# Kernel tuning notes

Hardware: AMD Instinct MI355X
Metric: run time of the kernel (lower is better)

Reference implementation:

```python
import jax, jax.numpy as jnp
import numpy as np

B, N_LAT, N_PAT = 32, 64, 4096
DIM_LAT = DIM_PAT = DIM_ATTN = 192
H = 6
HD = DIM_ATTN // H  # 32
SCALE = HD ** -0.5


def setup_inputs() -> dict:
    key = jax.random.key(0)
    ks = jax.random.split(key, 8)
    s = lambda fan_in: 1.0 / np.sqrt(fan_in)
    return {
        "x_latents": jax.random.normal(ks[0], (B, N_LAT, DIM_LAT), jnp.float32),
        "x_patches": jax.random.normal(ks[1], (B, N_PAT, DIM_PAT), jnp.float32),
        # weights stored [in, out] (torch Linear applies x @ W.T; math identical)
        "W_rv_lat": jax.random.uniform(ks[2], (DIM_LAT, 2 * DIM_ATTN), jnp.float32, -s(DIM_LAT), s(DIM_LAT)),
        "W_rv_pat": jax.random.uniform(ks[3], (DIM_PAT, 2 * DIM_ATTN), jnp.float32, -s(DIM_PAT), s(DIM_PAT)),
        "W_proj_lat": jax.random.uniform(ks[4], (DIM_ATTN, DIM_LAT), jnp.float32, -s(DIM_ATTN), s(DIM_ATTN)),
        "b_proj_lat": jax.random.uniform(ks[5], (DIM_LAT,), jnp.float32, -s(DIM_ATTN), s(DIM_ATTN)),
        "W_proj_pat": jax.random.uniform(ks[6], (DIM_ATTN, DIM_PAT), jnp.float32, -s(DIM_ATTN), s(DIM_ATTN)),
        "b_proj_pat": jax.random.uniform(ks[7], (DIM_PAT,), jnp.float32, -s(DIM_ATTN), s(DIM_ATTN)),
    }


def _split_rv(x, W, n):
    # x: [B, n, d_in] -> r, v each [B, H, n, HD]
    rv = (x @ W).reshape(x.shape[0], n, 2, H, HD)
    rv = jnp.transpose(rv, (2, 0, 3, 1, 4))  # [2, B, H, n, HD]
    return rv[0], rv[1]


def reference(x_latents, x_patches, W_rv_lat, W_rv_pat,
              W_proj_lat, b_proj_lat, W_proj_pat, b_proj_pat):
    r_lat, v_lat = _split_rv(x_latents, W_rv_lat, N_LAT)   # [B,H,N_lat,HD]
    r_pat, v_pat = _split_rv(x_patches, W_rv_pat, N_PAT)   # [B,H,N_pat,HD]

    # single score matrix, softmaxed along both axes (dropout = 0, eval mode)
    scores = jnp.einsum('bhld,bhpd->bhlp', r_lat, r_pat) * SCALE  # [B,H,N_lat,N_pat]
    attn = jax.nn.softmax(scores, axis=-1)    # row-wise (over patches)
    attn_T = jax.nn.softmax(scores, axis=-2)  # col-wise (over latents)

    out_lat = jnp.einsum('bhlp,bhpd->blhd', attn, v_pat).reshape(B, N_LAT, DIM_ATTN)
    out_pat = jnp.einsum('bhlp,bhld->bphd', attn_T, v_lat).reshape(B, N_PAT, DIM_ATTN)

    out_lat = out_lat @ W_proj_lat + b_proj_lat
    out_pat = out_pat @ W_proj_pat + b_proj_pat
    return out_lat, out_pat
```

## Files before the change

kernel.cpp:

```cpp
#include <hip/hip_runtime.h>

#define B_   32
#define NL_  64
#define NP_  4096
#define DIM_ 192
#define H_   6
#define HD_  32
#define PC_  128
#define NCH_ (NP_/PC_)
#define CPB_ 4
#define NSC_ (NCH_/CPB_)

typedef unsigned short u16;
typedef __attribute__((ext_vector_type(8))) short bf16x8;
typedef __attribute__((ext_vector_type(4))) short bf16x4;
typedef __attribute__((ext_vector_type(4))) float f32x4;

#define MFMA16(a,b,c) __builtin_amdgcn_mfma_f32_16x16x32_bf16(a,b,c,0,0,0)

__device__ __forceinline__ float bf2f(u16 s){ return __builtin_bit_cast(float,(unsigned)s<<16); }
__device__ __forceinline__ u16 f2bf(float f){
  unsigned u = __builtin_bit_cast(unsigned,f);
  return (u16)((u + 0x7FFFu + ((u>>16)&1u))>>16);
}

__global__ void k0_transpose(const float* __restrict__ W0, const float* __restrict__ W1,
                             const float* __restrict__ W2, const float* __restrict__ W3,
                             u16* __restrict__ T0, u16* __restrict__ T1,
                             u16* __restrict__ T2, u16* __restrict__ T3){
  int m = blockIdx.x >> 4, sub = blockIdx.x & 15;
  const float* src; u16* dst; int R, C;
  if      (m==0){src=W0;dst=T0;R=192;C=384;}
  else if (m==1){src=W1;dst=T1;R=192;C=384;}
  else if (m==2){src=W2;dst=T2;R=192;C=192;}
  else          {src=W3;dst=T3;R=192;C=192;}
  int total = R*C;
  for (int o = sub*256 + threadIdx.x; o < total; o += 16*256){
    int c = o / R, r = o - c*R;
    dst[o] = f2bf(src[r*C + c]);
  }
}

__global__ __launch_bounds__(256) void k_rv(const float* __restrict__ X,
    const u16* __restrict__ Wt, u16* __restrict__ R, u16* __restrict__ V,
    int Nseq, int nshift){
  __shared__ u16 As[128*200];
  __shared__ u16 Bs[64*200];
  const int t = threadIdx.x;
  const int m0 = blockIdx.x*128;
  const int lane = t & 63, w = t >> 6, g = lane >> 4, ln = lane & 15;
  const int srow = t >> 2, sc = (t & 3) * 8;
  const int bq = t & 3;
  const f32x4 ZF = {0.f,0.f,0.f,0.f};

  #pragma unroll
  for (int rr = 0; rr < 128; rr += 64){
    #pragma unroll
    for (int k0 = 0; k0 < 192; k0 += 32){
      float4 x0 = *(const float4*)&X[(size_t)(m0 + rr + srow)*192 + k0 + sc];
      float4 x1 = *(const float4*)&X[(size_t)(m0 + rr + srow)*192 + k0 + sc + 4];
      bf16x8 av;
      av[0]=(short)f2bf(x0.x); av[1]=(short)f2bf(x0.y); av[2]=(short)f2bf(x0.z); av[3]=(short)f2bf(x0.w);
      av[4]=(short)f2bf(x1.x); av[5]=(short)f2bf(x1.y); av[6]=(short)f2bf(x1.z); av[7]=(short)f2bf(x1.w);
      *(bf16x8*)&As[(rr + srow)*200 + k0 + sc] = av;
    }
  }

  bf16x8 breg[6];
  #pragma unroll
  for (int it=0; it<6; it++)
    breg[it] = *(const bf16x8*)&Wt[(size_t)srow*192 + bq*48 + it*8];

  __syncthreads();

  for (int n0 = 0; n0 < 384; n0 += 64){
    #pragma unroll
    for (int it=0; it<6; it++)
      *(bf16x8*)&Bs[srow*200 + bq*48 + it*8] = breg[it];
    if (n0 < 320){
      #pragma unroll
      for (int it=0; it<6; it++)
        breg[it] = *(const bf16x8*)&Wt[(size_t)(n0 + 64 + srow)*192 + bq*48 + it*8];
    }
    __syncthreads();

    f32x4 acc[2][4];
    #pragma unroll
    for(int i=0;i<2;i++)
      #pragma unroll
      for(int j=0;j<4;j++) acc[i][j]=ZF;
    #pragma unroll
    for (int k0 = 0; k0 < 192; k0 += 32){
      bf16x8 a0 = *(const bf16x8*)&As[(w*32      + ln)*200 + k0 + g*8];
      bf16x8 a1 = *(const bf16x8*)&As[(w*32 + 16 + ln)*200 + k0 + g*8];
      #pragma unroll
      for(int j=0;j<4;j++){
        bf16x8 bv = *(const bf16x8*)&Bs[(j*16 + ln)*200 + k0 + g*8];
        acc[0][j] = MFMA16(a0,bv,acc[0][j]);
        acc[1][j] = MFMA16(a1,bv,acc[1][j]);
      }
    }
    __syncthreads();

    #pragma unroll
    for(int i=0;i<2;i++)
      #pragma unroll
      for(int j=0;j<4;j++){
        int n = n0 + j*16 + ln;
        u16* dst; int c;
        if (n < 192){ dst = R; c = n; } else { dst = V; c = n - 192; }
        int h = c >> 5, d = c & 31;
        #pragma unroll
        for(int r=0;r<4;r++){
          int m = m0 + w*32 + i*16 + g*4 + r;
          int b = m >> nshift, sidx = m & (Nseq-1);
          dst[((((size_t)b*H_ + h)*(size_t)Nseq + sidx) << 5) + d] = f2bf(acc[i][j][r]);
        }
      }
  }
}

__global__ __launch_bounds__(256) void k_attn(
    const u16* __restrict__ r_lat_g, const u16* __restrict__ v_lat_g,
    const u16* __restrict__ r_pat_g, const u16* __restrict__ v_pat_g,
    u16* __restrict__ Opat,
    float* __restrict__ numT_ws,
    float* __restrict__ rowsum_ws){
  const float SCALE = 0.17677669529663687f;
  const int sc = blockIdx.x, h = blockIdx.y, b = blockIdx.z;
  const int bh = b*H_ + h;
  const int t = threadIdx.x, lane = t&63, w = t>>6, g = lane>>4, ln = lane&15;
  __shared__ u16 RL [64*40];
  __shared__ u16 VLT[32*72];
  __shared__ u16 EN [128*72];
  __shared__ u16 ET [64*136];
  __shared__ float RS[4*64];
  __shared__ u16 POOL[128*40];
  u16* RP  = POOL;
  u16* VPT = POOL;
  const f32x4 ZF = {0.f,0.f,0.f,0.f};

  const size_t latbase = (size_t)bh * (NL_*HD_);
  { int row = t>>2, col = (t&3)*8;
    *(bf16x8*)&RL[row*40+col] = *(const bf16x8*)&r_lat_g[latbase + row*32 + col]; }
  { int l = t>>2, dd = (t&3)*8;
    bf16x8 v = *(const bf16x8*)&v_lat_g[latbase + l*32 + dd];
    #pragma unroll
    for(int jj=0;jj<8;jj++) VLT[(dd+jj)*72 + l] = (u16)v[jj]; }

  const int p0 = t>>2, dd0 = (t&3)*8;
  const size_t pb0 = ((size_t)bh*NP_ + (size_t)sc*(CPB_*PC_))*HD_;
  bf16x8 rcur0 = *(const bf16x8*)&r_pat_g[pb0 + (size_t)p0*32 + dd0];
  bf16x8 rcur1 = *(const bf16x8*)&r_pat_g[pb0 + (size_t)(64+p0)*32 + dd0];
  bf16x8 vcur0 = *(const bf16x8*)&v_pat_g[pb0 + (size_t)p0*32 + dd0];
  bf16x8 vcur1 = *(const bf16x8*)&v_pat_g[pb0 + (size_t)(64+p0)*32 + dd0];

  f32x4 nm[2]; nm[0]=ZF; nm[1]=ZF;
  float rs[4] = {0.f,0.f,0.f,0.f};

  for (int c = 0; c < CPB_; ++c){
    *(bf16x8*)&RP[p0*40 + dd0]      = rcur0;
    *(bf16x8*)&RP[(64+p0)*40 + dd0] = rcur1;
    __syncthreads();

    f32x4 sf[2][4];
    { bf16x8 a0 = *(const bf16x8*)&RP[(w*32      + ln)*40 + g*8];
      bf16x8 a1 = *(const bf16x8*)&RP[(w*32 + 16 + ln)*40 + g*8];
      #pragma unroll
      for(int j=0;j<4;j++){
        bf16x8 bl = *(const bf16x8*)&RL[(j*16 + ln)*40 + g*8];
        sf[0][j] = MFMA16(a0, bl, ZF);
        sf[1][j] = MFMA16(a1, bl, ZF);
      } }

    bf16x8 rnxt0, rnxt1, vnxt0, vnxt1;
    const bool more = (c+1 < CPB_);
    if (more){
      const size_t pbn = pb0 + (size_t)(c+1)*(PC_*HD_);
      rnxt0 = *(const bf16x8*)&r_pat_g[pbn + (size_t)p0*32 + dd0];
      rnxt1 = *(const bf16x8*)&r_pat_g[pbn + (size_t)(64+p0)*32 + dd0];
      vnxt0 = *(const bf16x8*)&v_pat_g[pbn + (size_t)p0*32 + dd0];
      vnxt1 = *(const bf16x8*)&v_pat_g[pbn + (size_t)(64+p0)*32 + dd0];
    }

    float e[2][4][4], rcs[2][4];
    #pragma unroll
    for(int i=0;i<2;i++)
      #pragma unroll
      for(int r=0;r<4;r++){
        float cs = 0.f;
        #pragma unroll
        for(int j=0;j<4;j++){
          float ev = __expf(sf[i][j][r] * SCALE);
          e[i][j][r] = ev; cs += ev; rs[j] += ev;
        }
        cs += __shfl_xor(cs,1); cs += __shfl_xor(cs,2);
        cs += __shfl_xor(cs,4); cs += __shfl_xor(cs,8);
        rcs[i][r] = 1.0f / cs;
      }
    #pragma unroll
    for(int i=0;i<2;i++)
      #pragma unroll
      for(int j=0;j<4;j++){
        #pragma unroll
        for(int r=0;r<4;r++)
          EN[(w*32 + i*16 + g*4 + r)*72 + j*16 + ln] = f2bf(e[i][j][r]*rcs[i][r]);
        bf16x4 pk;
        #pragma unroll
        for(int r=0;r<4;r++) pk[r] = (short)f2bf(e[i][j][r]);
        *(bf16x4*)&ET[(j*16+ln)*136 + w*32 + i*16 + g*4] = pk;
      }
    __syncthreads();

    #pragma unroll
    for(int jj=0;jj<8;jj++){
      VPT[(dd0+jj)*136 + p0]      = (u16)vcur0[jj];
      VPT[(dd0+jj)*136 + 64 + p0] = (u16)vcur1[jj];
    }

    f32x4 op[2][2];
    #pragma unroll
    for(int i=0;i<2;i++){ op[i][0]=ZF; op[i][1]=ZF; }
    #pragma unroll
    for(int ks=0; ks<2; ks++){
      bf16x8 bv[2];
      #pragma unroll
      for(int jd=0;jd<2;jd++) bv[jd] = *(const bf16x8*)&VLT[(jd*16+ln)*72 + ks*32 + g*8];
      #pragma unroll
      for(int i=0;i<2;i++){
        bf16x8 af = *(const bf16x8*)&EN[(w*32 + i*16 + ln)*72 + ks*32 + g*8];
        #pragma unroll
        for(int jd=0;jd<2;jd++) op[i][jd] = MFMA16(af, bv[jd], op[i][jd]);
      }
    }
    const size_t obase = ((size_t)b*NP_ + (size_t)(sc*CPB_ + c)*PC_)*DIM_ + h*32;
    #pragma unroll
    for(int i=0;i<2;i++)
      #pragma unroll
      for(int jd=0;jd<2;jd++)
        #pragma unroll
        for(int r=0;r<4;r++){
          int p = w*32 + i*16 + g*4 + r, dd = jd*16 + ln;
          Opat[obase + (size_t)p*DIM_ + dd] = f2bf(op[i][jd][r]);
        }
    __syncthreads();

    #pragma unroll
    for(int ks=0; ks<4; ks++){
      bf16x8 af = *(const bf16x8*)&ET[(w*16+ln)*136 + ks*32 + g*8];
      #pragma unroll
      for(int dj=0;dj<2;dj++){
        bf16x8 bv = *(const bf16x8*)&VPT[(dj*16+ln)*136 + ks*32 + g*8];
        nm[dj] = MFMA16(af, bv, nm[dj]);
      }
    }
    __syncthreads();

    if (more){ rcur0=rnxt0; rcur1=rnxt1; vcur0=vnxt0; vcur1=vnxt1; }
  }

  #pragma unroll
  for(int j=0;j<4;j++){
    float vs = rs[j];
    vs += __shfl_xor(vs,16); vs += __shfl_xor(vs,32);
    if (g == 0) RS[w*64 + j*16 + ln] = vs;
  }
  __syncthreads();
  if (t < 64)
    rowsum_ws[((size_t)bh*NSC_ + sc)*64 + t] = RS[t] + RS[64+t] + RS[128+t] + RS[192+t];
  float* dstN = numT_ws + ((size_t)bh*NSC_ + sc)*2048;
  #pragma unroll
  for(int dj=0;dj<2;dj++)
    #pragma unroll
    for(int r=0;r<4;r++){
      int l = w*16 + g*4 + r, dd = dj*16 + ln;
      dstN[l*32 + dd] = nm[dj][r];
    }
}

__global__ __launch_bounds__(256) void k_lat_reduce(const float* __restrict__ numT_ws,
    const float* __restrict__ rowsum_ws, u16* __restrict__ attn_lat){
  int bh = blockIdx.x, b = bh / H_, h = bh - b*H_;
  __shared__ float RSs[64];
  int t = threadIdx.x;
  if (t < 64){
    float s = 0.f;
    for(int c=0;c<NSC_;c++) s += rowsum_ws[((size_t)bh*NSC_ + c)*64 + t];
    RSs[t] = 1.0f / s;
  }
  __syncthreads();
  for(int idx = t; idx < 2048; idx += 256){
    int l = idx >> 5, dd = idx & 31;
    float s = 0.f;
    for(int c=0;c<NSC_;c++) s += numT_ws[((size_t)bh*NSC_ + c)*2048 + idx];
    attn_lat[((size_t)b*NL_ + l)*DIM_ + h*32 + dd] = f2bf(s * RSs[l]);
  }
}

__global__ __launch_bounds__(256) void k_proj_lat(const u16* __restrict__ A,
    const u16* __restrict__ Wt, const float* __restrict__ bias, float* __restrict__ out){
  int b = blockIdx.x;
  __shared__ u16 As[64*40];
  __shared__ u16 Bs[192*40];
  int t = threadIdx.x, lane = t&63, w = t>>6, g = lane>>4, ln = lane&15;
  const f32x4 ZF = {0.f,0.f,0.f,0.f};
  f32x4 acc[4][3];
  #pragma unroll
  for(int i=0;i<4;i++)
    #pragma unroll
    for(int j=0;j<3;j++) acc[i][j]=ZF;
  for(int k0=0;k0<192;k0+=32){
    bf16x8 av; bf16x8 bv[3];
    { int row = t>>2, col=(t&3)*8;
      av = *(const bf16x8*)&A[((size_t)b*NL_ + row)*DIM_ + k0 + col]; }
    #pragma unroll
    for(int it=0;it<3;it++){
      int e = it*2048 + t*8, row = e>>5, col = (t&3)*8;
      bv[it] = *(const bf16x8*)&Wt[(size_t)row*192 + k0 + col];
    }
    if (k0) __syncthreads();
    { int row = t>>2, col=(t&3)*8; *(bf16x8*)&As[row*40+col] = av; }
    #pragma unroll
    for(int it=0;it<3;it++){
      int e = it*2048 + t*8, row = e>>5, col = (t&3)*8;
      *(bf16x8*)&Bs[row*40+col] = bv[it];
    }
    __syncthreads();
    bf16x8 bw[3];
    #pragma unroll
    for(int jf=0;jf<3;jf++) bw[jf] = *(const bf16x8*)&Bs[(w*48 + jf*16 + ln)*40 + g*8];
    #pragma unroll
    for(int lf=0;lf<4;lf++){
      bf16x8 af = *(const bf16x8*)&As[(lf*16 + ln)*40 + g*8];
      #pragma unroll
      for(int jf=0;jf<3;jf++) acc[lf][jf] = MFMA16(af, bw[jf], acc[lf][jf]);
    }
  }
  #pragma unroll
  for(int lf=0;lf<4;lf++)
    #pragma unroll
    for(int jf=0;jf<3;jf++){
      int j = w*48 + jf*16 + ln;
      float bs = bias[j];
      #pragma unroll
      for(int r=0;r<4;r++){
        int l = lf*16 + g*4 + r;
        out[((size_t)b*NL_ + l)*DIM_ + j] = acc[lf][jf][r] + bs;
      }
    }
}

__global__ __launch_bounds__(256) void k_proj_pat(const u16* __restrict__ X,
    const u16* __restrict__ Wt, const float* __restrict__ bias, float* __restrict__ out){
  __shared__ u16 As[64*40];
  __shared__ u16 Bs[64*40];
  const int t = threadIdx.x;
  const int m0 = blockIdx.x*64, n0 = blockIdx.y*64;
  const int lane = t & 63, w = t >> 6, g = lane >> 4, ln = lane & 15;
  const int wr = w >> 1, wc = w & 1;
  const int srow = t >> 2, scol = (t & 3) * 8;
  const f32x4 ZF = {0.f,0.f,0.f,0.f};
  f32x4 acc[2][2];
  #pragma unroll
  for(int i=0;i<2;i++){ acc[i][0]=ZF; acc[i][1]=ZF; }
  for (int k0 = 0; k0 < 192; k0 += 32){
    bf16x8 av = *(const bf16x8*)&X [(size_t)(m0 + srow)*192 + k0 + scol];
    bf16x8 bv = *(const bf16x8*)&Wt[(size_t)(n0 + srow)*192 + k0 + scol];
    if (k0) __syncthreads();
    *(bf16x8*)&As[srow*40 + scol] = av;
    *(bf16x8*)&Bs[srow*40 + scol] = bv;
    __syncthreads();
    bf16x8 a0 = *(const bf16x8*)&As[(wr*32      + ln)*40 + g*8];
    bf16x8 a1 = *(const bf16x8*)&As[(wr*32 + 16 + ln)*40 + g*8];
    bf16x8 b0 = *(const bf16x8*)&Bs[(wc*32      + ln)*40 + g*8];
    bf16x8 b1 = *(const bf16x8*)&Bs[(wc*32 + 16 + ln)*40 + g*8];
    acc[0][0] = MFMA16(a0,b0,acc[0][0]);
    acc[0][1] = MFMA16(a0,b1,acc[0][1]);
    acc[1][0] = MFMA16(a1,b0,acc[1][0]);
    acc[1][1] = MFMA16(a1,b1,acc[1][1]);
  }
  #pragma unroll
  for(int i=0;i<2;i++)
    #pragma unroll
    for(int j=0;j<2;j++){
      int n = n0 + wc*32 + j*16 + ln;
      float bs = bias[n];
      #pragma unroll
      for(int r=0;r<4;r++){
        int m = m0 + wr*32 + i*16 + g*4 + r;
        out[(size_t)m*192 + n] = acc[i][j][r] + bs;
      }
    }
}

extern "C" void kernel_launch(void* const* d_in, const int* in_sizes, int n_in,
                              void* d_out, int out_size, void* d_ws, size_t ws_size,
                              hipStream_t stream){
  const float* x_lat  = (const float*)d_in[0];
  const float* x_pat  = (const float*)d_in[1];
  const float* W_rv_l = (const float*)d_in[2];
  const float* W_rv_p = (const float*)d_in[3];
  const float* W_pj_l = (const float*)d_in[4];
  const float* b_pj_l = (const float*)d_in[5];
  const float* W_pj_p = (const float*)d_in[6];
  const float* b_pj_p = (const float*)d_in[7];
  float* out = (float*)d_out;

  char* ws = (char*)d_ws;
  size_t off = 0;
  auto alloc = [&](size_t bytes)->void*{ void* p = ws + off; off += (bytes + 255) & ~(size_t)255; return p; };
  u16* WtRL   = (u16*)alloc((size_t)384*192*2);
  u16* WtRP   = (u16*)alloc((size_t)384*192*2);
  u16* WtPL   = (u16*)alloc((size_t)192*192*2);
  u16* WtPP   = (u16*)alloc((size_t)192*192*2);
  u16* r_lat  = (u16*)alloc((size_t)B_*H_*NL_*HD_*2);
  u16* v_lat  = (u16*)alloc((size_t)B_*H_*NL_*HD_*2);
  u16* r_pat  = (u16*)alloc((size_t)B_*H_*NP_*HD_*2);
  u16* v_pat  = (u16*)alloc((size_t)B_*H_*NP_*HD_*2);
  u16* Opat   = (u16*)alloc((size_t)B_*NP_*DIM_*2);
  float* numT = (float*)alloc((size_t)B_*H_*NSC_*64*32*4);
  float* rsum = (float*)alloc((size_t)B_*H_*NSC_*64*4);
  u16* attn_l = (u16*)alloc((size_t)B_*NL_*DIM_*2);

  k0_transpose<<<64,256,0,stream>>>(W_rv_l, W_rv_p, W_pj_l, W_pj_p, WtRL, WtRP, WtPL, WtPP);
  k_rv<<<dim3((B_*NP_)/128),256,0,stream>>>(x_pat, WtRP, r_pat, v_pat, NP_, 12);
  k_rv<<<dim3((B_*NL_)/128),256,0,stream>>>(x_lat, WtRL, r_lat, v_lat, NL_, 6);
  k_attn<<<dim3(NSC_, H_, B_),256,0,stream>>>(r_lat, v_lat, r_pat, v_pat, Opat, numT, rsum);
  k_lat_reduce<<<B_*H_,256,0,stream>>>(numT, rsum, attn_l);
  k_proj_lat<<<B_,256,0,stream>>>(attn_l, WtPL, b_pj_l, out);
  k_proj_pat<<<dim3((B_*NP_)/64, 3),256,0,stream>>>(Opat, WtPP, b_pj_p, out + (size_t)B_*NL_*DIM_);
}
```

Before: 190.0 us.

## Use 512-thread blocks for rv projection and restructure patch projection tiling

k_rv now runs with 512 threads (8 waves), each wave computing a 16-row slice instead of 32 rows, so more waves share the same LDS tiles. k_proj_pat is rewritten to stage a full 128x192 activation tile in LDS once and loop over the three 64-column weight slabs with register-prefetched weights, replacing the 3-way grid split that reloaded activations per column block. This cuts redundant activation reads and per-k synchronisation, but uses far more LDS per block, which may reduce occupancy.

Result: faster. 184.6 us (-2.9%).

```diff
diff --git a/kernel.cpp b/kernel.cpp
--- a/kernel.cpp
+++ b/kernel.cpp
@@ -41,7 +41,7 @@
   }
 }
 
-__global__ __launch_bounds__(256) void k_rv(const float* __restrict__ X,
+__global__ __launch_bounds__(512) void k_rv(const float* __restrict__ X,
     const u16* __restrict__ Wt, u16* __restrict__ R, u16* __restrict__ V,
     int Nseq, int nshift){
   __shared__ u16 As[128*200];
@@ -50,73 +50,64 @@
   const int m0 = blockIdx.x*128;
   const int lane = t & 63, w = t >> 6, g = lane >> 4, ln = lane & 15;
   const int srow = t >> 2, sc = (t & 3) * 8;
-  const int bq = t & 3;
+  const int srB = t >> 3, bq = t & 7;
   const f32x4 ZF = {0.f,0.f,0.f,0.f};
 
   #pragma unroll
-  for (int rr = 0; rr < 128; rr += 64){
+  for (int k0 = 0; k0 < 192; k0 += 32){
+    float4 x0 = *(const float4*)&X[(size_t)(m0 + srow)*192 + k0 + sc];
+    float4 x1 = *(const float4*)&X[(size_t)(m0 + srow)*192 + k0 + sc + 4];
+    bf16x8 av;
+    av[0]=(short)f2bf(x0.x); av[1]=(short)f2bf(x0.y); av[2]=(short)f2bf(x0.z); av[3]=(short)f2bf(x0.w);
+    av[4]=(short)f2bf(x1.x); av[5]=(short)f2bf(x1.y); av[6]=(short)f2bf(x1.z); av[7]=(short)f2bf(x1.w);
+    *(bf16x8*)&As[srow*200 + k0 + sc] = av;
+  }
+
+  bf16x8 breg[3];
+  #pragma unroll
+  for (int it=0; it<3; it++)
+    breg[it] = *(const bf16x8*)&Wt[(size_t)srB*192 + bq*24 + it*8];
+
+  __syncthreads();
+
+  for (int n0 = 0; n0 < 384; n0 += 64){
+    #pragma unroll
+    for (int it=0; it<3; it++)
+      *(bf16x8*)&Bs[srB*200 + bq*24 + it*8] = breg[it];
+    if (n0 < 320){
+      #pragma unroll
+      for (int it=0; it<3; it++)
+        breg[it] = *(const bf16x8*)&Wt[(size_t)(n0 + 64 + srB)*192 + bq*24 + it*8];
+    }
+    __syncthreads();
+
+    f32x4 acc[4];
+    #pragma unroll
+    for(int j=0;j<4;j++) acc[j]=ZF;
     #pragma unroll
     for (int k0 = 0; k0 < 192; k0 += 32){
-      float4 x0 = *(const float4*)&X[(size_t)(m0 + rr + srow)*192 + k0 + sc];
-      float4 x1 = *(const float4*)&X[(size_t)(m0 + rr + srow)*192 + k0 + sc + 4];
-      bf16x8 av;
-      av[0]=(short)f2bf(x0.x); av[1]=(short)f2bf(x0.y); av[2]=(short)f2bf(x0.z); av[3]=(short)f2bf(x0.w);
-      av[4]=(short)f2bf(x1.x); av[5]=(short)f2bf(x1.y); av[6]=(short)f2bf(x1.z); av[7]=(short)f2bf(x1.w);
-      *(bf16x8*)&As[(rr + srow)*200 + k0 + sc] = av;
-    }
-  }
-
-  bf16x8 breg[6];
-  #pragma unroll
-  for (int it=0; it<6; it++)
-    breg[it] = *(const bf16x8*)&Wt[(size_t)srow*192 + bq*48 + it*8];
-
-  __syncthreads();
-
-  for (int n0 = 0; n0 < 384; n0 += 64){
-    #pragma unroll
-    for (int it=0; it<6; it++)
-      *(bf16x8*)&Bs[srow*200 + bq*48 + it*8] = breg[it];
-    if (n0 < 320){
-      #pragma unroll
-      for (int it=0; it<6; it++)
-        breg[it] = *(const bf16x8*)&Wt[(size_t)(n0 + 64 + srow)*192 + bq*48 + it*8];
-    }
-    __syncthreads();
-
-    f32x4 acc[2][4];
-    #pragma unroll
-    for(int i=0;i<2;i++)
-      #pragma unroll
-      for(int j=0;j<4;j++) acc[i][j]=ZF;
-    #pragma unroll
-    for (int k0 = 0; k0 < 192; k0 += 32){
-      bf16x8 a0 = *(const bf16x8*)&As[(w*32      + ln)*200 + k0 + g*8];
-      bf16x8 a1 = *(const bf16x8*)&As[(w*32 + 16 + ln)*200 + k0 + g*8];
+      bf16x8 a0 = *(const bf16x8*)&As[(w*16 + ln)*200 + k0 + g*8];
       #pragma unroll
       for(int j=0;j<4;j++){
         bf16x8 bv = *(const bf16x8*)&Bs[(j*16 + ln)*200 + k0 + g*8];
-        acc[0][j] = MFMA16(a0,bv,acc[0][j]);
-        acc[1][j] = MFMA16(a1,bv,acc[1][j]);
-      }
-    }
-    __syncthreads();
-
-    #pragma unroll
-    for(int i=0;i<2;i++)
-      #pragma unroll
-      for(int j=0;j<4;j++){
-        int n = n0 + j*16 + ln;
-        u16* dst; int c;
-        if (n < 192){ dst = R; c = n; } else { dst = V; c = n - 192; }
-        int h = c >> 5, d = c & 31;
-        #pragma unroll
-        for(int r=0;r<4;r++){
-          int m = m0 + w*32 + i*16 + g*4 + r;
-          int b = m >> nshift, sidx = m & (Nseq-1);
-          dst[((((size_t)b*H_ + h)*(size_t)Nseq + sidx) << 5) + d] = f2bf(acc[i][j][r]);
-        }
-      }
+        acc[j] = MFMA16(a0,bv,acc[j]);
+      }
+    }
+    __syncthreads();
+
+    #pragma unroll
+    for(int j=0;j<4;j++){
+      int n = n0 + j*16 + ln;
+      u16* dst; int c;
+      if (n < 192){ dst = R; c = n; } else { dst = V; c = n - 192; }
+      int h = c >> 5, d = c & 31;
+      #pragma unroll
+      for(int r=0;r<4;r++){
+        int m = m0 + w*16 + g*4 + r;
+        int b = m >> nshift, sidx = m & (Nseq-1);
+        dst[((((size_t)b*H_ + h)*(size_t)Nseq + sidx) << 5) + d] = f2bf(acc[j][r]);
+      }
+    }
   }
 }
 
@@ -350,47 +341,64 @@
     }
 }
 
-__global__ __launch_bounds__(256) void k_proj_pat(const u16* __restrict__ X,
+__global__ __launch_bounds__(512) void k_proj_pat(const u16* __restrict__ X,
     const u16* __restrict__ Wt, const float* __restrict__ bias, float* __restrict__ out){
-  __shared__ u16 As[64*40];
-  __shared__ u16 Bs[64*40];
+  __shared__ u16 As[128*200];
+  __shared__ u16 Bs[64*200];
   const int t = threadIdx.x;
-  const int m0 = blockIdx.x*64, n0 = blockIdx.y*64;
+  const int m0 = blockIdx.x*128;
   const int lane = t & 63, w = t >> 6, g = lane >> 4, ln = lane & 15;
-  const int wr = w >> 1, wc = w & 1;
-  const int srow = t >> 2, scol = (t & 3) * 8;
+  const int srow = t >> 2, sc = (t & 3) * 8;
+  const int srB = t >> 3, bq = t & 7;
   const f32x4 ZF = {0.f,0.f,0.f,0.f};
-  f32x4 acc[2][2];
-  #pragma unroll
-  for(int i=0;i<2;i++){ acc[i][0]=ZF; acc[i][1]=ZF; }
-  for (int k0 = 0; k0 < 192; k0 += 32){
-    bf16x8 av = *(const bf16x8*)&X [(size_t)(m0 + srow)*192 + k0 + scol];
-    bf16x8 bv = *(const bf16x8*)&Wt[(size_t)(n0 + srow)*192 + k0 + scol];
-    if (k0) __syncthreads();
-    *(bf16x8*)&As[srow*40 + scol] = av;
-    *(bf16x8*)&Bs[srow*40 + scol] = bv;
-    __syncthreads();
-    bf16x8 a0 = *(const bf16x8*)&As[(wr*32      + ln)*40 + g*8];
-    bf16x8 a1 = *(const bf16x8*)&As[(wr*32 + 16 + ln)*40 + g*8];
-    bf16x8 b0 = *(const bf16x8*)&Bs[(wc*32      + ln)*40 + g*8];
-    bf16x8 b1 = *(const bf16x8*)&Bs[(wc*32 + 16 + ln)*40 + g*8];
-    acc[0][0] = MFMA16(a0,b0,acc[0][0]);
-    acc[0][1] = MFMA16(a0,b1,acc[0][1]);
-    acc[1][0] = MFMA16(a1,b0,acc[1][0]);
-    acc[1][1] = MFMA16(a1,b1,acc[1][1]);
-  }
-  #pragma unroll
-  for(int i=0;i<2;i++)
-    #pragma unroll
-    for(int j=0;j<2;j++){
-      int n = n0 + wc*32 + j*16 + ln;
+
+  #pragma unroll
+  for (int k0 = 0; k0 < 192; k0 += 32)
+    *(bf16x8*)&As[srow*200 + k0 + sc] = *(const bf16x8*)&X[(size_t)(m0 + srow)*192 + k0 + sc];
+
+  bf16x8 breg[3];
+  #pragma unroll
+  for (int it=0; it<3; it++)
+    breg[it] = *(const bf16x8*)&Wt[(size_t)srB*192 + bq*24 + it*8];
+
+  __syncthreads();
+
+  for (int n0 = 0; n0 < 192; n0 += 64){
+    #pragma unroll
+    for (int it=0; it<3; it++)
+      *(bf16x8*)&Bs[srB*200 + bq*24 + it*8] = breg[it];
+    if (n0 < 128){
+      #pragma unroll
+      for (int it=0; it<3; it++)
+        breg[it] = *(const bf16x8*)&Wt[(size_t)(n0 + 64 + srB)*192 + bq*24 + it*8];
+    }
+    __syncthreads();
+
+    f32x4 acc[4];
+    #pragma unroll
+    for(int j=0;j<4;j++) acc[j]=ZF;
+    #pragma unroll
+    for (int k0 = 0; k0 < 192; k0 += 32){
+      bf16x8 a0 = *(const bf16x8*)&As[(w*16 + ln)*200 + k0 + g*8];
+      #pragma unroll
+      for(int j=0;j<4;j++){
+        bf16x8 bv = *(const bf16x8*)&Bs[(j*16 + ln)*200 + k0 + g*8];
+        acc[j] = MFMA16(a0,bv,acc[j]);
+      }
+    }
+    __syncthreads();
+
+    #pragma unroll
+    for(int j=0;j<4;j++){
+      int n = n0 + j*16 + ln;
       float bs = bias[n];
       #pragma unroll
       for(int r=0;r<4;r++){
-        int m = m0 + wr*32 + i*16 + g*4 + r;
-        out[(size_t)m*192 + n] = acc[i][j][r] + bs;
-      }
-    }
+        int m = m0 + w*16 + g*4 + r;
+        out[(size_t)m*192 + n] = acc[j][r] + bs;
+      }
+    }
+  }
 }
 
 extern "C" void kernel_launch(void* const* d_in, const int* in_sizes, int n_in,
@@ -423,10 +431,10 @@
   u16* attn_l = (u16*)alloc((size_t)B_*NL_*DIM_*2);
 
   k0_transpose<<<64,256,0,stream>>>(W_rv_l, W_rv_p, W_pj_l, W_pj_p, WtRL, WtRP, WtPL, WtPP);
-  k_rv<<<dim3((B_*NP_)/128),256,0,stream>>>(x_pat, WtRP, r_pat, v_pat, NP_, 12);
-  k_rv<<<dim3((B_*NL_)/128),256,0,stream>>>(x_lat, WtRL, r_lat, v_lat, NL_, 6);
+  k_rv<<<dim3((B_*NP_)/128),512,0,stream>>>(x_pat, WtRP, r_pat, v_pat, NP_, 12);
+  k_rv<<<dim3((B_*NL_)/128),512,0,stream>>>(x_lat, WtRL, r_lat, v_lat, NL_, 6);
   k_attn<<<dim3(NSC_, H_, B_),256,0,stream>>>(r_lat, v_lat, r_pat, v_pat, Opat, numT, rsum);
   k_lat_reduce<<<B_*H_,256,0,stream>>>(numT, rsum, attn_l);
   k_proj_lat<<<B_,256,0,stream>>>(attn_l, WtPL, b_pj_l, out);
-  k_proj_pat<<<dim3((B_*NP_)/64, 3),256,0,stream>>>(Opat, WtPP, b_pj_p, out + (size_t)B_*NL_*DIM_);
-}
+  k_proj_pat<<<dim3((B_*NP_)/128),512,0,stream>>>(Opat, WtPP, b_pj_p, out + (size_t)B_*NL_*DIM_);
+}
```
